# Optimization experiments

Hardware: AMD Instinct MI355X
Metric: run time of the kernel (lower is better)

The kernel has to match this reference:

```python
import jax, jax.numpy as jnp
import numpy as np

DN = ('NCHW', 'OIHW', 'NCHW')

def conv3x3(x, w):
    return jax.lax.conv_general_dilated(x, w, (1, 1), [(1, 1), (1, 1)], dimension_numbers=DN)

def setup_inputs() -> dict:
    key = jax.random.key(0)
    ks = jax.random.split(key, 5)
    N, C, H, W = 64, 512, 16, 16
    fan = C * 3 * 3
    s = 1.0 / np.sqrt(fan)
    x = jax.random.normal(ks[0], (N, C, H, W), dtype=jnp.float32)
    Wq = jax.random.normal(ks[1], (C, C, 3, 3), dtype=jnp.float32) * s
    Wk = jax.random.normal(ks[2], (C, C, 3, 3), dtype=jnp.float32) * s
    Wv = jax.random.normal(ks[3], (C, C, 3, 3), dtype=jnp.float32) * s
    Wc = jax.random.normal(ks[4], (C, C, 3, 3), dtype=jnp.float32) * s
    gamma = jnp.ones((C,), dtype=jnp.float32)
    beta = jnp.zeros((C,), dtype=jnp.float32)
    return {"x": x, "Wq": Wq, "Wk": Wk, "Wv": Wv, "Wc": Wc, "gamma": gamma, "beta": beta}

def reference(x, Wq, Wk, Wv, Wc, gamma, beta):
    C = x.shape[1]
    q = conv3x3(x, Wq)  # [N,C,H,W]
    k = conv3x3(x, Wk)
    v = conv3x3(x, Wv)
    # att[n,m,h,w] = sum_c q[n,c,h,w] * k[m,c,h,w] / sqrt(C); softmax over m
    att = jnp.einsum('nchw,mchw->nmhw', q, k) / jnp.sqrt(jnp.float32(C))
    att = jax.nn.softmax(att, axis=1)
    # virt[n,c,h,w] = sum_m att[n,m,h,w] * v[m,c,h,w]
    virt = jnp.einsum('nmhw,mchw->nchw', att, v)
    # GroupNorm(1, C): normalize over (C,H,W) per sample, per-channel affine
    mu = jnp.mean(virt, axis=(1, 2, 3), keepdims=True)
    var = jnp.var(virt, axis=(1, 2, 3), keepdims=True)
    virt = (virt - mu) * jax.lax.rsqrt(var + 1e-5)
    virt = virt * gamma[None, :, None, None] + beta[None, :, None, None]
    virt = jax.nn.relu(virt)
    virt = conv3x3(virt, Wc)
    # Dropout is identity in eval mode
    return x + virt
```

## Files before the change

### kernel.cpp

```cpp
#include <hip/hip_runtime.h>
#include <math.h>

typedef unsigned short u16;
typedef unsigned int u32;
typedef short short8 __attribute__((ext_vector_type(8)));
typedef float f32x4 __attribute__((ext_vector_type(4)));

#define NB 64
#define CCH 512
#define HW 256

__device__ __forceinline__ u16 f2bf(float f) {
    union { float f; u32 u; } x; x.f = f;
    u32 r = x.u + 0x7fffu + ((x.u >> 16) & 1u);
    return (u16)(r >> 16);
}
__device__ __forceinline__ float bf2f(u16 b) {
    union { u32 u; float f; } x; x.u = ((u32)b) << 16;
    return x.f;
}
__device__ __forceinline__ void gload_lds16(const u16* g, u16* l) {
    __builtin_amdgcn_global_load_lds((const __attribute__((address_space(1))) u32*)g,
                                     (__attribute__((address_space(3))) u32*)l, 16, 0, 0);
}

__global__ __launch_bounds__(256) void zero_borders(u16* __restrict__ pad) {
    const int n = blockIdx.x, t = threadIdx.x;
    short8 z = (short8){0,0,0,0,0,0,0,0};
    for (int idx = t; idx < 68 * 64; idx += 256) {
        int cell = idx >> 6, ch = idx & 63;
        int hh, ww;
        if (cell < 18)      { hh = 0;          ww = cell; }
        else if (cell < 36) { hh = 17;         ww = cell - 18; }
        else if (cell < 52) { hh = cell - 35;  ww = 0; }
        else                { hh = cell - 51;  ww = 17; }
        *(short8*)(pad + ((size_t)((n * 18 + hh) * 18 + ww)) * 512 + ch * 8) = z;
    }
}

__global__ __launch_bounds__(256) void prep_x(const float* __restrict__ x, u16* __restrict__ pad) {
    __shared__ float tl[64][65];
    const int n = blockIdx.z, c0 = blockIdx.y * 64, p0 = blockIdx.x * 64;
    const int t = threadIdx.x;
    {
        const int cc = t >> 2, ps = (t & 3) * 16;
#pragma unroll
        for (int i = 0; i < 4; ++i) {
            float4 v4 = *(const float4*)(x + (((size_t)(n * 512 + c0 + cc)) << 8) + p0 + ps + i * 4);
            tl[cc][ps + i * 4 + 0] = v4.x;
            tl[cc][ps + i * 4 + 1] = v4.y;
            tl[cc][ps + i * 4 + 2] = v4.z;
            tl[cc][ps + i * 4 + 3] = v4.w;
        }
    }
    __syncthreads();
    {
        const int pp = t >> 2, cs = (t & 3) * 16;
        short8 o0, o1;
#pragma unroll
        for (int i = 0; i < 8; ++i) o0[i] = (short)f2bf(tl[cs + i][pp]);
#pragma unroll
        for (int i = 0; i < 8; ++i) o1[i] = (short)f2bf(tl[cs + 8 + i][pp]);
        const int p = p0 + pp, h = p >> 4, wcol = p & 15;
        u16* dst = pad + ((size_t)((n * 18 + h + 1) * 18 + wcol + 1)) * 512 + c0 + cs;
        *(short8*)(dst + 0) = o0;
        *(short8*)(dst + 8) = o1;
    }
}

__global__ __launch_bounds__(256) void prep_w(
    const float* __restrict__ Wq, const float* __restrict__ Wk,
    const float* __restrict__ Wv, const float* __restrict__ Wc,
    u16* __restrict__ Wt)
{
    __shared__ float lw[4608];
    const int co = blockIdx.x, sel = blockIdx.y, t = threadIdx.x;
    const float* Ws = (sel == 0) ? Wq : (sel == 1) ? Wk : (sel == 2) ? Wv : Wc;
#pragma unroll
    for (int i = 0; i < 18; ++i) lw[t + i * 256] = Ws[(size_t)co * 4608 + t + i * 256];
    __syncthreads();
    for (int tap = 0; tap < 9; ++tap)
#pragma unroll
        for (int hh = 0; hh < 2; ++hh) {
            int ci = t + hh * 256;
            Wt[(((size_t)(sel * 9 + tap)) << 18) + (co << 9) + ci] = f2bf(lw[ci * 9 + tap]);
        }
}

__global__ __launch_bounds__(512, 1) void qkv_mfma8(
    const u16* __restrict__ pad, const u16* __restrict__ Wt,
    u16* __restrict__ q, u16* __restrict__ k, u16* __restrict__ v)
{
    __shared__ short As[3][8192];
    __shared__ short Bs[3][6144];
    const int t = threadIdx.x;
    const int l = t & 63;
    const int wid = t >> 6;
    const int wm = wid >> 2, wn = wid & 3;

    const int o = blockIdx.x;
    const int wg = (o & 7) * 64 + (o >> 3);
    const int imbase = (wg >> 3) * 256;
    const int cobase = (wg & 7) * 192;

    const int cl = ((l & 3) - ((l >> 3) & 3)) & 3;
    int imoffA[2], woffB[2];
#pragma unroll
    for (int rr = 0; rr < 2; ++rr) {
        const int chunk = wid * 2 + rr;
        const int imrow = imbase + chunk * 16 + (l >> 2);
        const int p = imrow >> 6, n = imrow & 63;
        imoffA[rr] = ((n * 18 + (p >> 4)) * 18 + (p & 15)) * 512 + cl * 8;
        const int cof = cobase + chunk * 16 + (l >> 2);
        const int sel = cof >> 9, co = cof & 511;
        woffB[rr] = sel * 9 * 262144 + co * 512 + cl * 8;
    }

    const int fp = ((l >> 4) + (l >> 1)) & 3;
    const int aoff = (wm * 128 + (l & 15)) * 32 + fp * 8;
    const int boff = (wn * 48 + (l & 15)) * 32 + fp * 8;

    f32x4 acc[8][3];
#pragma unroll
    for (int i = 0; i < 8; ++i)
#pragma unroll
        for (int j = 0; j < 3; ++j) acc[i][j] = (f32x4){0.f, 0.f, 0.f, 0.f};

    auto STAGE_A = [&](int kt, int s) {
        const int tap = kt >> 4;
        const int shift = ((tap / 3) * 18 + (tap % 3)) * 512 + (kt & 15) * 32;
#pragma unroll
        for (int rr = 0; rr < 2; ++rr)
            gload_lds16(pad + imoffA[rr] + shift, (u16*)(&As[s][0] + (wid * 2 + rr) * 512));
    };
    auto STAGE_B = [&](int kt, int s) {
        if (wid < 6) {
            const int tap = kt >> 4;
            const int shift = tap * 262144 + (kt & 15) * 32;
#pragma unroll
            for (int rr = 0; rr < 2; ++rr)
                gload_lds16(Wt + woffB[rr] + shift, (u16*)(&Bs[s][0] + (wid * 2 + rr) * 512));
        }
    };

    STAGE_A(0, 0); STAGE_B(0, 0);
    STAGE_A(1, 1); STAGE_B(1, 1);

    int s0 = 0;
    short8 fa0[4], fa1[4], fb[3];
#pragma unroll 1
    for (int kt = 0; kt < 144; ++kt) {
        const int s2 = (s0 == 0) ? 2 : s0 - 1;
        const short* Ab = &As[s0][0];
        const short* Bb = &Bs[s0][0];

        if (kt == 143) {
            asm volatile("s_waitcnt vmcnt(0)" ::: "memory");
        } else if (wid < 6) {
            asm volatile("s_waitcnt vmcnt(4)" ::: "memory");
        } else {
            asm volatile("s_waitcnt vmcnt(2)" ::: "memory");
        }
        __builtin_amdgcn_sched_barrier(0);
        __builtin_amdgcn_s_barrier();
        __builtin_amdgcn_sched_barrier(0);

#pragma unroll
        for (int j = 0; j < 3; ++j) fb[j] = *(const short8*)(Bb + boff + j * 512);
#pragma unroll
        for (int i = 0; i < 4; ++i) fa0[i] = *(const short8*)(Ab + aoff + i * 512);
#pragma unroll
        for (int i = 0; i < 4; ++i) fa1[i] = *(const short8*)(Ab + aoff + 2048 + i * 512);

        if (kt < 142) { STAGE_A(kt + 2, s2); STAGE_B(kt + 2, s2); }

        __builtin_amdgcn_s_setprio(1);
#pragma unroll
        for (int i = 0; i < 4; ++i)
#pragma unroll
            for (int j = 0; j < 3; ++j)
                acc[i][j] = __builtin_amdgcn_mfma_f32_16x16x32_bf16(fa0[i], fb[j], acc[i][j], 0, 0, 0);
#pragma unroll
        for (int i = 0; i < 4; ++i)
#pragma unroll
            for (int j = 0; j < 3; ++j)
                acc[4 + i][j] = __builtin_amdgcn_mfma_f32_16x16x32_bf16(fa1[i], fb[j], acc[4 + i][j], 0, 0, 0);
        __builtin_amdgcn_s_setprio(0);

        s0 = (s0 == 2) ? 0 : s0 + 1;
    }

#pragma unroll
    for (int j = 0; j < 3; ++j) {
        const int colb = cobase + wn * 48 + j * 16;
        u16* op = ((colb >> 9) == 0) ? q : (((colb >> 9) == 1) ? k : v);
        op += (colb & 511) + (l & 15);
#pragma unroll
        for (int i = 0; i < 8; ++i) {
            const int row = imbase + wm * 128 + i * 16 + (l >> 4) * 4;
#pragma unroll
            for (int r = 0; r < 4; ++r)
                op[(size_t)(row + r) * 512] = f2bf(acc[i][j][r]);
        }
    }
}

__global__ __launch_bounds__(256, 2) void cres_mfma(
    const u16* __restrict__ pad, const u16* __restrict__ Wt,
    const float* __restrict__ xres, float* __restrict__ out)
{
    __shared__ short bufA[2][4096];
    __shared__ short bufB[2][4096];
    const int t = threadIdx.x;
    const int l = t & 63;
    const int w = t >> 6;
    const int wr = w >> 1, wc = w & 1;

    const int imbase = blockIdx.x * 128;
    const int cobase = blockIdx.y * 128;

    const int lr = l >> 2;
    const int cl = ((l & 3) - ((l >> 3) & 3)) & 3;
    int imoff[2], woff[2];
#pragma unroll
    for (int i = 0; i < 2; ++i) {
        int r = w * 32 + i * 16 + lr;
        int imrow = imbase + r;
        int n = imrow >> 8, p = imrow & 255;
        int h = p >> 4, wco = p & 15;
        imoff[i] = ((n * 18 + h) * 18 + wco) * 512 + cl * 8;
        woff[i]  = (cobase + r) * 512 + cl * 8;
    }
    const int fragoff = (l & 15) * 32 + ((((l >> 4) + (l >> 1)) & 3)) * 8;

    f32x4 acc[4][4];
#pragma unroll
    for (int a = 0; a < 4; ++a)
#pragma unroll
        for (int b = 0; b < 4; ++b) acc[a][b] = (f32x4){0.f, 0.f, 0.f, 0.f};

    auto STAGE = [&](int s, int j, int k0) {
        const int shift = ((j / 3) * 18 + (j % 3)) * 512 + k0;
        const size_t wjo = ((size_t)j << 18) + k0;
#pragma unroll
        for (int i = 0; i < 2; ++i) {
            gload_lds16(pad + imoff[i] + shift, (u16*)&bufA[s][(w * 32 + i * 16) * 32]);
            gload_lds16(Wt + woff[i]  + wjo,   (u16*)&bufB[s][(w * 32 + i * 16) * 32]);
        }
    };

    STAGE(0, 0, 0);
    __syncthreads();

    for (int kt = 0; kt < 144; ++kt) {
        const int cur = kt & 1;
        if (kt < 143) {
            const int kn = kt + 1;
            STAGE(cur ^ 1, kn >> 4, (kn & 15) * 32);
        }
        short8 fa[4], fb[4];
        const short* IMb = &bufA[cur][0];
        const short* Wb  = &bufB[cur][0];
#pragma unroll
        for (int f = 0; f < 4; ++f) {
            const int imr = wc * 64 + f * 16;
            const int wrr = wr * 64 + f * 16;
            fb[f] = *(const short8*)(IMb + imr * 32 + fragoff);
            fa[f] = *(const short8*)(Wb  + wrr * 32 + fragoff);
        }
#pragma unroll
        for (int fm = 0; fm < 4; ++fm)
#pragma unroll
            for (int fn = 0; fn < 4; ++fn)
                acc[fm][fn] = __builtin_amdgcn_mfma_f32_16x16x32_bf16(fa[fm], fb[fn], acc[fm][fn], 0, 0, 0);
        __syncthreads();
    }

#pragma unroll
    for (int fm = 0; fm < 4; ++fm)
#pragma unroll
        for (int fn = 0; fn < 4; ++fn)
#pragma unroll
            for (int r = 0; r < 4; ++r) {
                int co = cobase + wr * 64 + fm * 16 + (l >> 4) * 4 + r;
                int imrow = imbase + wc * 64 + fn * 16 + (l & 15);
                int n = imrow >> 8, p = imrow & 255;
                size_t addr = (((size_t)(n * 512 + co)) << 8) + p;
                out[addr] = acc[fm][fn][r] + xres[addr];
            }
}

__global__ __launch_bounds__(256) void attn_kernel(
    const u16* __restrict__ qT, const u16* __restrict__ kT, u16* vvT)
{
    const int p = blockIdx.x;
    const int t = threadIdx.x;
    __shared__ float smemA[2][64][68];
    __shared__ float attb[64][68];
    const size_t pb = (size_t)p * (NB * CCH);

    const int ng = t >> 4, mg = t & 15;
    const int n0 = ng * 4, m0 = mg * 4;
    float acc[4][4];
#pragma unroll
    for (int i = 0; i < 4; ++i)
#pragma unroll
        for (int j = 0; j < 4; ++j) acc[i][j] = 0.f;

    for (int ct = 0; ct < 8; ++ct) {
        const int c0 = ct * 64;
        __syncthreads();
#pragma unroll
        for (int s = 0; s < 2; ++s) {
            int f = t + s * 256;
            int nn = f >> 3, c8 = (f & 7) * 8;
            short8 qv = *(const short8*)(qT + pb + (size_t)nn * CCH + c0 + c8);
            short8 kv = *(const short8*)(kT + pb + (size_t)nn * CCH + c0 + c8);
#pragma unroll
            for (int e = 0; e < 8; ++e) {
                smemA[0][nn][c8 + e] = bf2f((u16)qv[e]);
                smemA[1][nn][c8 + e] = bf2f((u16)kv[e]);
            }
        }
        __syncthreads();
#pragma unroll 4
        for (int c4 = 0; c4 < 16; ++c4) {
            float4 q4[4], k4[4];
#pragma unroll
            for (int i = 0; i < 4; ++i) q4[i] = *(const float4*)&smemA[0][n0 + i][c4 * 4];
#pragma unroll
            for (int j = 0; j < 4; ++j) k4[j] = *(const float4*)&smemA[1][m0 + j][c4 * 4];
#pragma unroll
            for (int i = 0; i < 4; ++i)
#pragma unroll
                for (int j = 0; j < 4; ++j) {
                    acc[i][j] = fmaf(q4[i].x, k4[j].x, acc[i][j]);
                    acc[i][j] = fmaf(q4[i].y, k4[j].y, acc[i][j]);
                    acc[i][j] = fmaf(q4[i].z, k4[j].z, acc[i][j]);
                    acc[i][j] = fmaf(q4[i].w, k4[j].w, acc[i][j]);
                }
        }
    }

    const float SCALE = 0.0441941738241592f;
#pragma unroll
    for (int i = 0; i < 4; ++i) {
        float m = fmaxf(fmaxf(acc[i][0], acc[i][1]), fmaxf(acc[i][2], acc[i][3]));
#pragma unroll
        for (int mask = 1; mask < 16; mask <<= 1) m = fmaxf(m, __shfl_xor(m, mask, 16));
        float e[4]; float s = 0.f;
#pragma unroll
        for (int j = 0; j < 4; ++j) { e[j] = __expf((acc[i][j] - m) * SCALE); s += e[j]; }
#pragma unroll
        for (int mask = 1; mask < 16; mask <<= 1) s += __shfl_xor(s, mask, 16);
        float inv = 1.f / s;
#pragma unroll
        for (int j = 0; j < 4; ++j) attb[n0 + i][m0 + j] = e[j] * inv;
    }
    __syncthreads();

    float* vs = &smemA[0][0][0];
    const int ng2 = t >> 3, cg = t & 7;
    const int nn0 = ng2 * 2, cb = cg * 16;
    for (int ct4 = 0; ct4 < 4; ++ct4) {
        const int c0 = ct4 * 128;
#pragma unroll
        for (int s = 0; s < 4; ++s) {
            int f = t + s * 256;
            int m = f >> 4, c8 = (f & 15) * 8;
            short8 vv = *(const short8*)(vvT + pb + (size_t)m * CCH + c0 + c8);
#pragma unroll
            for (int e = 0; e < 8; ++e) vs[m * 132 + c8 + e] = bf2f((u16)vv[e]);
        }
        __syncthreads();
        float acc2[2][16];
#pragma unroll
        for (int i = 0; i < 2; ++i)
#pragma unroll
            for (int j = 0; j < 16; ++j) acc2[i][j] = 0.f;
#pragma unroll 4
        for (int m = 0; m < 64; ++m) {
            float a0 = attb[nn0][m], a1 = attb[nn0 + 1][m];
#pragma unroll
            for (int k4 = 0; k4 < 4; ++k4) {
                float4 v4 = *(const float4*)&vs[m * 132 + cb + k4 * 4];
                acc2[0][k4 * 4 + 0] = fmaf(a0, v4.x, acc2[0][k4 * 4 + 0]);
                acc2[0][k4 * 4 + 1] = fmaf(a0, v4.y, acc2[0][k4 * 4 + 1]);
                acc2[0][k4 * 4 + 2] = fmaf(a0, v4.z, acc2[0][k4 * 4 + 2]);
                acc2[0][k4 * 4 + 3] = fmaf(a0, v4.w, acc2[0][k4 * 4 + 3]);
                acc2[1][k4 * 4 + 0] = fmaf(a1, v4.x, acc2[1][k4 * 4 + 0]);
                acc2[1][k4 * 4 + 1] = fmaf(a1, v4.y, acc2[1][k4 * 4 + 1]);
                acc2[1][k4 * 4 + 2] = fmaf(a1, v4.z, acc2[1][k4 * 4 + 2]);
                acc2[1][k4 * 4 + 3] = fmaf(a1, v4.w, acc2[1][k4 * 4 + 3]);
            }
        }
#pragma unroll
        for (int i = 0; i < 2; ++i)
#pragma unroll
            for (int j = 0; j < 16; ++j)
                vvT[pb + (size_t)(nn0 + i) * CCH + c0 + cb + j] = f2bf(acc2[i][j]);
        __syncthreads();
    }
}

__global__ __launch_bounds__(256) void gn_kernel(
    const u16* __restrict__ virtT, const float* __restrict__ gamma,
    const float* __restrict__ beta, u16* __restrict__ ypad)
{
    const int n = blockIdx.x, t = threadIdx.x;
    __shared__ float sg[512], sb[512];
    for (int i = t; i < 512; i += 256) { sg[i] = gamma[i]; sb[i] = beta[i]; }

    float sum = 0.f, ss = 0.f;
    for (int it = 0; it < 64; ++it) {
        int f = t + it * 256;
        int p = f >> 6, c = (f & 63) * 8;
        short8 vv = *(const short8*)(virtT + ((size_t)(p * 64 + n)) * 512 + c);
#pragma unroll
        for (int e = 0; e < 8; ++e) { float x = bf2f((u16)vv[e]); sum += x; ss = fmaf(x, x, ss); }
    }
#pragma unroll
    for (int off = 32; off > 0; off >>= 1) {
        sum += __shfl_down(sum, off);
        ss  += __shfl_down(ss, off);
    }
    __shared__ float rs[4], rss[4], stats[2];
    const int wid = t >> 6, lane = t & 63;
    if (lane == 0) { rs[wid] = sum; rss[wid] = ss; }
    __syncthreads();
    if (t == 0) {
        float S = rs[0] + rs[1] + rs[2] + rs[3];
        float SS = rss[0] + rss[1] + rss[2] + rss[3];
        float mu = S * (1.f / 131072.f);
        float var = SS * (1.f / 131072.f) - mu * mu;
        stats[0] = mu;
        stats[1] = rsqrtf(var + 1e-5f);
    }
    __syncthreads();
    const float mu = stats[0], rstd = stats[1];

    for (int it = 0; it < 64; ++it) {
        int f = t + it * 256;
        int p = f >> 6, cc = (f & 63) * 8;
        short8 vv = *(const short8*)(virtT + ((size_t)(p * 64 + n)) * 512 + cc);
        short8 ov;
#pragma unroll
        for (int e = 0; e < 8; ++e) {
            float x = (bf2f((u16)vv[e]) - mu) * rstd;
            x = fmaf(x, sg[cc + e], sb[cc + e]);
            ov[e] = (short)f2bf(fmaxf(x, 0.f));
        }
        int h = p >> 4, wcol = p & 15;
        *(short8*)(ypad + ((size_t)((n * 18 + h + 1) * 18 + wcol + 1)) * 512 + cc) = ov;
    }
}

extern "C" void kernel_launch(void* const* d_in, const int* in_sizes, int n_in,
                              void* d_out, int out_size, void* d_ws, size_t ws_size,
                              hipStream_t stream)
{
    const float* x     = (const float*)d_in[0];
    const float* Wq    = (const float*)d_in[1];
    const float* Wk    = (const float*)d_in[2];
    const float* Wv    = (const float*)d_in[3];
    const float* Wc    = (const float*)d_in[4];
    const float* gamma = (const float*)d_in[5];
    const float* beta  = (const float*)d_in[6];
    float* out = (float*)d_out;

    u16* pad = (u16*)d_ws;
    u16* Wt  = pad + 10616832;
    u16* q   = Wt + 9437184;
    u16* k   = q + 8388608;
    u16* v   = k + 8388608;

    zero_borders<<<dim3(64), dim3(256), 0, stream>>>(pad);
    prep_x<<<dim3(4, 8, 64), dim3(256), 0, stream>>>(x, pad);
    prep_w<<<dim3(512, 4), dim3(256), 0, stream>>>(Wq, Wk, Wv, Wc, Wt);

    qkv_mfma8<<<dim3(512), dim3(512), 0, stream>>>(pad, Wt, q, k, v);
    attn_kernel<<<dim3(256), dim3(256), 0, stream>>>(q, k, v);
    gn_kernel<<<dim3(64), dim3(256), 0, stream>>>(v, gamma, beta, pad);
    cres_mfma<<<dim3(128, 4), dim3(256), 0, stream>>>(pad, Wt + 3 * 2359296, x, out);
}
```

Baseline: 427.8 us.

## Deepen GEMM pipelines, register double-buffer fragments, split GroupNorm across more blocks

The QKV conv GEMM moves from a 3-stage to a 4-stage LDS pipeline and double-buffers fragments in registers so LDS reads for the next k-step overlap the current MFMAs. The output conv is rewritten as a 512-thread, 256x128-tile kernel with the same 4-stage prefetch scheme, replacing the 2-stage 128x128 version. GroupNorm is split into a partial-sum kernel and a normalize kernel, each using 256 blocks instead of 64, to raise parallelism. This costs more LDS and registers per block plus one extra launch, and it reuses the k buffer as scratch for the partial sums.

Result: faster. 399.0 us (-6.7%).

```diff
diff --git a/kernel.cpp b/kernel.cpp
--- a/kernel.cpp
+++ b/kernel.cpp
@@ -91,8 +91,8 @@
     const u16* __restrict__ pad, const u16* __restrict__ Wt,
     u16* __restrict__ q, u16* __restrict__ k, u16* __restrict__ v)
 {
-    __shared__ short As[3][8192];
-    __shared__ short Bs[3][6144];
+    __shared__ short As[4][8192];
+    __shared__ short Bs[4][6144];
     const int t = threadIdx.x;
     const int l = t & 63;
     const int wid = t >> 6;
@@ -145,50 +145,53 @@
 
     STAGE_A(0, 0); STAGE_B(0, 0);
     STAGE_A(1, 1); STAGE_B(1, 1);
-
-    int s0 = 0;
-    short8 fa0[4], fa1[4], fb[3];
+    STAGE_A(2, 2); STAGE_B(2, 2);
+    if (wid < 6) asm volatile("s_waitcnt vmcnt(8)" ::: "memory");
+    else         asm volatile("s_waitcnt vmcnt(4)" ::: "memory");
+    __builtin_amdgcn_sched_barrier(0);
+    __builtin_amdgcn_s_barrier();
+    __builtin_amdgcn_sched_barrier(0);
+
+    short8 A0[8], A1[8], B0[3], B1[3];
+#pragma unroll
+    for (int j = 0; j < 3; ++j) B0[j] = *(const short8*)(&Bs[0][0] + boff + j * 512);
+#pragma unroll
+    for (int i = 0; i < 8; ++i) A0[i] = *(const short8*)(&As[0][0] + aoff + i * 512);
+
+#define QSTEP(KT, BUFR, BUFS, AM, BMF, AR, BRF)                                   \
+    {                                                                             \
+        if ((KT) >= 142)  asm volatile("s_waitcnt vmcnt(0)" ::: "memory");        \
+        else if (wid < 6) asm volatile("s_waitcnt vmcnt(4)" ::: "memory");        \
+        else              asm volatile("s_waitcnt vmcnt(2)" ::: "memory");        \
+        __builtin_amdgcn_sched_barrier(0);                                        \
+        __builtin_amdgcn_s_barrier();                                             \
+        __builtin_amdgcn_sched_barrier(0);                                        \
+        if ((KT) < 143) {                                                         \
+            const short* Abr = &As[BUFR][0];                                      \
+            const short* Bbr = &Bs[BUFR][0];                                      \
+            _Pragma("unroll")                                                     \
+            for (int j = 0; j < 3; ++j) BRF[j] = *(const short8*)(Bbr + boff + j * 512); \
+            _Pragma("unroll")                                                     \
+            for (int i = 0; i < 8; ++i) AR[i] = *(const short8*)(Abr + aoff + i * 512);  \
+        }                                                                         \
+        if ((KT) + 3 < 144) { STAGE_A((KT) + 3, BUFS); STAGE_B((KT) + 3, BUFS); } \
+        __builtin_amdgcn_s_setprio(1);                                            \
+        _Pragma("unroll")                                                         \
+        for (int i = 0; i < 8; ++i)                                               \
+            _Pragma("unroll")                                                     \
+            for (int j = 0; j < 3; ++j)                                           \
+                acc[i][j] = __builtin_amdgcn_mfma_f32_16x16x32_bf16(AM[i], BMF[j], acc[i][j], 0, 0, 0); \
+        __builtin_amdgcn_s_setprio(0);                                            \
+    }
+
 #pragma unroll 1
-    for (int kt = 0; kt < 144; ++kt) {
-        const int s2 = (s0 == 0) ? 2 : s0 - 1;
-        const short* Ab = &As[s0][0];
-        const short* Bb = &Bs[s0][0];
-
-        if (kt == 143) {
-            asm volatile("s_waitcnt vmcnt(0)" ::: "memory");
-        } else if (wid < 6) {
-            asm volatile("s_waitcnt vmcnt(4)" ::: "memory");
-        } else {
-            asm volatile("s_waitcnt vmcnt(2)" ::: "memory");
-        }
-        __builtin_amdgcn_sched_barrier(0);
-        __builtin_amdgcn_s_barrier();
-        __builtin_amdgcn_sched_barrier(0);
-
-#pragma unroll
-        for (int j = 0; j < 3; ++j) fb[j] = *(const short8*)(Bb + boff + j * 512);
-#pragma unroll
-        for (int i = 0; i < 4; ++i) fa0[i] = *(const short8*)(Ab + aoff + i * 512);
-#pragma unroll
-        for (int i = 0; i < 4; ++i) fa1[i] = *(const short8*)(Ab + aoff + 2048 + i * 512);
-
-        if (kt < 142) { STAGE_A(kt + 2, s2); STAGE_B(kt + 2, s2); }
-
-        __builtin_amdgcn_s_setprio(1);
-#pragma unroll
-        for (int i = 0; i < 4; ++i)
-#pragma unroll
-            for (int j = 0; j < 3; ++j)
-                acc[i][j] = __builtin_amdgcn_mfma_f32_16x16x32_bf16(fa0[i], fb[j], acc[i][j], 0, 0, 0);
-#pragma unroll
-        for (int i = 0; i < 4; ++i)
-#pragma unroll
-            for (int j = 0; j < 3; ++j)
-                acc[4 + i][j] = __builtin_amdgcn_mfma_f32_16x16x32_bf16(fa1[i], fb[j], acc[4 + i][j], 0, 0, 0);
-        __builtin_amdgcn_s_setprio(0);
-
-        s0 = (s0 == 2) ? 0 : s0 + 1;
-    }
+    for (int kt = 0; kt < 144; kt += 4) {
+        QSTEP(kt + 0, 1, 3, A0, B0, A1, B1);
+        QSTEP(kt + 1, 2, 0, A1, B1, A0, B0);
+        QSTEP(kt + 2, 3, 1, A0, B0, A1, B1);
+        QSTEP(kt + 3, 0, 2, A1, B1, A0, B0);
+    }
+#undef QSTEP
 
 #pragma unroll
     for (int j = 0; j < 3; ++j) {
@@ -205,88 +208,116 @@
     }
 }
 
-__global__ __launch_bounds__(256, 2) void cres_mfma(
-    const u16* __restrict__ pad, const u16* __restrict__ Wt,
+__global__ __launch_bounds__(512, 1) void cres_pipe(
+    const u16* __restrict__ pad, const u16* __restrict__ WtC,
     const float* __restrict__ xres, float* __restrict__ out)
 {
-    __shared__ short bufA[2][4096];
-    __shared__ short bufB[2][4096];
+    __shared__ short As[4][4096];
+    __shared__ short Bs[4][8192];
     const int t = threadIdx.x;
     const int l = t & 63;
-    const int w = t >> 6;
-    const int wr = w >> 1, wc = w & 1;
-
-    const int imbase = blockIdx.x * 128;
-    const int cobase = blockIdx.y * 128;
-
-    const int lr = l >> 2;
+    const int wid = t >> 6;
+    const int wm = wid >> 2, wn = wid & 3;
+
+    const int cobase = (blockIdx.x & 3) * 128;
+    const int imbase = (blockIdx.x >> 2) * 256;
+
     const int cl = ((l & 3) - ((l >> 3) & 3)) & 3;
-    int imoff[2], woff[2];
-#pragma unroll
-    for (int i = 0; i < 2; ++i) {
-        int r = w * 32 + i * 16 + lr;
-        int imrow = imbase + r;
-        int n = imrow >> 8, p = imrow & 255;
-        int h = p >> 4, wco = p & 15;
-        imoff[i] = ((n * 18 + h) * 18 + wco) * 512 + cl * 8;
-        woff[i]  = (cobase + r) * 512 + cl * 8;
-    }
-    const int fragoff = (l & 15) * 32 + ((((l >> 4) + (l >> 1)) & 3)) * 8;
+    int woffA, imoffB[2];
+    {
+        const int co = cobase + wid * 16 + (l >> 2);
+        woffA = co * 512 + cl * 8;
+    }
+#pragma unroll
+    for (int rr = 0; rr < 2; ++rr) {
+        const int u = wid * 2 + rr;
+        const int imrow = imbase + u * 16 + (l >> 2);
+        const int n = imrow >> 8, p = imrow & 255;
+        imoffB[rr] = ((n * 18 + (p >> 4)) * 18 + (p & 15)) * 512 + cl * 8;
+    }
+
+    const int fp = ((l >> 4) + (l >> 1)) & 3;
+    const int aoff = (wm * 64 + (l & 15)) * 32 + fp * 8;
+    const int boff = (wn * 64 + (l & 15)) * 32 + fp * 8;
 
     f32x4 acc[4][4];
 #pragma unroll
-    for (int a = 0; a < 4; ++a)
-#pragma unroll
-        for (int b = 0; b < 4; ++b) acc[a][b] = (f32x4){0.f, 0.f, 0.f, 0.f};
-
-    auto STAGE = [&](int s, int j, int k0) {
-        const int shift = ((j / 3) * 18 + (j % 3)) * 512 + k0;
-        const size_t wjo = ((size_t)j << 18) + k0;
-#pragma unroll
-        for (int i = 0; i < 2; ++i) {
-            gload_lds16(pad + imoff[i] + shift, (u16*)&bufA[s][(w * 32 + i * 16) * 32]);
-            gload_lds16(Wt + woff[i]  + wjo,   (u16*)&bufB[s][(w * 32 + i * 16) * 32]);
-        }
+    for (int i = 0; i < 4; ++i)
+#pragma unroll
+        for (int j = 0; j < 4; ++j) acc[i][j] = (f32x4){0.f, 0.f, 0.f, 0.f};
+
+    auto STAGE_CA = [&](int kt, int s) {
+        const int tap = kt >> 4;
+        const int shift = tap * 262144 + (kt & 15) * 32;
+        gload_lds16(WtC + woffA + shift, (u16*)(&As[s][0] + wid * 512));
     };
-
-    STAGE(0, 0, 0);
-    __syncthreads();
-
-    for (int kt = 0; kt < 144; ++kt) {
-        const int cur = kt & 1;
-        if (kt < 143) {
-            const int kn = kt + 1;
-            STAGE(cur ^ 1, kn >> 4, (kn & 15) * 32);
-        }
-        short8 fa[4], fb[4];
-        const short* IMb = &bufA[cur][0];
-        const short* Wb  = &bufB[cur][0];
-#pragma unroll
-        for (int f = 0; f < 4; ++f) {
-            const int imr = wc * 64 + f * 16;
-            const int wrr = wr * 64 + f * 16;
-            fb[f] = *(const short8*)(IMb + imr * 32 + fragoff);
-            fa[f] = *(const short8*)(Wb  + wrr * 32 + fragoff);
-        }
-#pragma unroll
-        for (int fm = 0; fm < 4; ++fm)
-#pragma unroll
-            for (int fn = 0; fn < 4; ++fn)
-                acc[fm][fn] = __builtin_amdgcn_mfma_f32_16x16x32_bf16(fa[fm], fb[fn], acc[fm][fn], 0, 0, 0);
-        __syncthreads();
-    }
-
-#pragma unroll
-    for (int fm = 0; fm < 4; ++fm)
-#pragma unroll
-        for (int fn = 0; fn < 4; ++fn)
+    auto STAGE_CB = [&](int kt, int s) {
+        const int tap = kt >> 4;
+        const int shift = ((tap / 3) * 18 + (tap % 3)) * 512 + (kt & 15) * 32;
+#pragma unroll
+        for (int rr = 0; rr < 2; ++rr)
+            gload_lds16(pad + imoffB[rr] + shift, (u16*)(&Bs[s][0] + (wid * 2 + rr) * 512));
+    };
+
+    STAGE_CA(0, 0); STAGE_CB(0, 0);
+    STAGE_CA(1, 1); STAGE_CB(1, 1);
+    STAGE_CA(2, 2); STAGE_CB(2, 2);
+    asm volatile("s_waitcnt vmcnt(6)" ::: "memory");
+    __builtin_amdgcn_sched_barrier(0);
+    __builtin_amdgcn_s_barrier();
+    __builtin_amdgcn_sched_barrier(0);
+
+    short8 A0[4], A1[4], B0[4], B1[4];
+#pragma unroll
+    for (int i = 0; i < 4; ++i) A0[i] = *(const short8*)(&As[0][0] + aoff + i * 512);
+#pragma unroll
+    for (int j = 0; j < 4; ++j) B0[j] = *(const short8*)(&Bs[0][0] + boff + j * 512);
+
+#define CSTEP(KT, BUFR, BUFS, AM, BMF, AR, BRF)                                   \
+    {                                                                             \
+        if ((KT) >= 142) asm volatile("s_waitcnt vmcnt(0)" ::: "memory");         \
+        else             asm volatile("s_waitcnt vmcnt(3)" ::: "memory");         \
+        __builtin_amdgcn_sched_barrier(0);                                        \
+        __builtin_amdgcn_s_barrier();                                             \
+        __builtin_amdgcn_sched_barrier(0);                                        \
+        if ((KT) < 143) {                                                         \
+            const short* Abr = &As[BUFR][0];                                      \
+            const short* Bbr = &Bs[BUFR][0];                                      \
+            _Pragma("unroll")                                                     \
+            for (int i = 0; i < 4; ++i) AR[i] = *(const short8*)(Abr + aoff + i * 512);  \
+            _Pragma("unroll")                                                     \
+            for (int j = 0; j < 4; ++j) BRF[j] = *(const short8*)(Bbr + boff + j * 512); \
+        }                                                                         \
+        if ((KT) + 3 < 144) { STAGE_CA((KT) + 3, BUFS); STAGE_CB((KT) + 3, BUFS); } \
+        __builtin_amdgcn_s_setprio(1);                                            \
+        _Pragma("unroll")                                                         \
+        for (int i = 0; i < 4; ++i)                                               \
+            _Pragma("unroll")                                                     \
+            for (int j = 0; j < 4; ++j)                                           \
+                acc[i][j] = __builtin_amdgcn_mfma_f32_16x16x32_bf16(AM[i], BMF[j], acc[i][j], 0, 0, 0); \
+        __builtin_amdgcn_s_setprio(0);                                            \
+    }
+
+#pragma unroll 1
+    for (int kt = 0; kt < 144; kt += 4) {
+        CSTEP(kt + 0, 1, 3, A0, B0, A1, B1);
+        CSTEP(kt + 1, 2, 0, A1, B1, A0, B0);
+        CSTEP(kt + 2, 3, 1, A0, B0, A1, B1);
+        CSTEP(kt + 3, 0, 2, A1, B1, A0, B0);
+    }
+#undef CSTEP
+
+#pragma unroll
+    for (int i = 0; i < 4; ++i)
+#pragma unroll
+        for (int j = 0; j < 4; ++j)
 #pragma unroll
             for (int r = 0; r < 4; ++r) {
-                int co = cobase + wr * 64 + fm * 16 + (l >> 4) * 4 + r;
-                int imrow = imbase + wc * 64 + fn * 16 + (l & 15);
+                int co = cobase + wm * 64 + i * 16 + (l >> 4) * 4 + r;
+                int imrow = imbase + wn * 64 + j * 16 + (l & 15);
                 int n = imrow >> 8, p = imrow & 255;
                 size_t addr = (((size_t)(n * 512 + co)) << 8) + p;
-                out[addr] = acc[fm][fn][r] + xres[addr];
+                out[addr] = acc[i][j][r] + xres[addr];
             }
 }
 
@@ -403,18 +434,15 @@
     }
 }
 
-__global__ __launch_bounds__(256) void gn_kernel(
-    const u16* __restrict__ virtT, const float* __restrict__ gamma,
-    const float* __restrict__ beta, u16* __restrict__ ypad)
-{
-    const int n = blockIdx.x, t = threadIdx.x;
-    __shared__ float sg[512], sb[512];
-    for (int i = t; i < 512; i += 256) { sg[i] = gamma[i]; sb[i] = beta[i]; }
-
+__global__ __launch_bounds__(256) void gn_part1(
+    const u16* __restrict__ virtT, float* __restrict__ partials)
+{
+    const int n = blockIdx.x >> 2, qr = blockIdx.x & 3, t = threadIdx.x;
     float sum = 0.f, ss = 0.f;
-    for (int it = 0; it < 64; ++it) {
+#pragma unroll 4
+    for (int it = 0; it < 16; ++it) {
         int f = t + it * 256;
-        int p = f >> 6, c = (f & 63) * 8;
+        int p = qr * 64 + (f >> 6), c = (f & 63) * 8;
         short8 vv = *(const short8*)(virtT + ((size_t)(p * 64 + n)) * 512 + c);
 #pragma unroll
         for (int e = 0; e < 8; ++e) { float x = bf2f((u16)vv[e]); sum += x; ss = fmaf(x, x, ss); }
@@ -424,24 +452,39 @@
         sum += __shfl_down(sum, off);
         ss  += __shfl_down(ss, off);
     }
-    __shared__ float rs[4], rss[4], stats[2];
+    __shared__ float rs[4], rss[4];
     const int wid = t >> 6, lane = t & 63;
     if (lane == 0) { rs[wid] = sum; rss[wid] = ss; }
     __syncthreads();
     if (t == 0) {
-        float S = rs[0] + rs[1] + rs[2] + rs[3];
-        float SS = rss[0] + rss[1] + rss[2] + rss[3];
-        float mu = S * (1.f / 131072.f);
-        float var = SS * (1.f / 131072.f) - mu * mu;
-        stats[0] = mu;
-        stats[1] = rsqrtf(var + 1e-5f);
-    }
+        partials[(n * 4 + qr) * 2 + 0] = rs[0] + rs[1] + rs[2] + rs[3];
+        partials[(n * 4 + qr) * 2 + 1] = rss[0] + rss[1] + rss[2] + rss[3];
+    }
+}
+
+__global__ __launch_bounds__(256) void gn_part2(
+    const u16* __restrict__ virtT, const float* __restrict__ partials,
+    const float* __restrict__ gamma, const float* __restrict__ beta,
+    u16* __restrict__ ypad)
+{
+    const int n = blockIdx.x >> 2, qr = blockIdx.x & 3, t = threadIdx.x;
+    __shared__ float sg[512], sb[512];
+    for (int i = t; i < 512; i += 256) { sg[i] = gamma[i]; sb[i] = beta[i]; }
+    float S = 0.f, SS = 0.f;
+#pragma unroll
+    for (int i = 0; i < 4; ++i) {
+        S  += partials[(n * 4 + i) * 2 + 0];
+        SS += partials[(n * 4 + i) * 2 + 1];
+    }
+    const float mu = S * (1.f / 131072.f);
+    const float var = SS * (1.f / 131072.f) - mu * mu;
+    const float rstd = rsqrtf(var + 1e-5f);
     __syncthreads();
-    const float mu = stats[0], rstd = stats[1];
-
-    for (int it = 0; it < 64; ++it) {
+
+#pragma unroll 4
+    for (int it = 0; it < 16; ++it) {
         int f = t + it * 256;
-        int p = f >> 6, cc = (f & 63) * 8;
+        int p = qr * 64 + (f >> 6), cc = (f & 63) * 8;
         short8 vv = *(const short8*)(virtT + ((size_t)(p * 64 + n)) * 512 + cc);
         short8 ov;
 #pragma unroll
@@ -473,6 +516,7 @@
     u16* q   = Wt + 9437184;
     u16* k   = q + 8388608;
     u16* v   = k + 8388608;
+    float* gnp = (float*)k;
 
     zero_borders<<<dim3(64), dim3(256), 0, stream>>>(pad);
     prep_x<<<dim3(4, 8, 64), dim3(256), 0, stream>>>(x, pad);
@@ -480,6 +524,7 @@
 
     qkv_mfma8<<<dim3(512), dim3(512), 0, stream>>>(pad, Wt, q, k, v);
     attn_kernel<<<dim3(256), dim3(256), 0, stream>>>(q, k, v);
-    gn_kernel<<<dim3(64), dim3(256), 0, stream>>>(v, gamma, beta, pad);
-    cres_mfma<<<dim3(128, 4), dim3(256), 0, stream>>>(pad, Wt + 3 * 2359296, x, out);
-}
+    gn_part1<<<dim3(256), dim3(256), 0, stream>>>(v, gnp);
+    gn_part2<<<dim3(256), dim3(256), 0, stream>>>(v, gnp, gamma, beta, pad);
+    cres_pipe<<<dim3(256), dim3(512), 0, stream>>>(pad, Wt + 3 * 2359296, x, out);
+}
```
